# Performance work log

Measured on AMD Instinct MI355X. Metric: run time of the kernel, lower is better.

## Reference

```python
import jax, jax.numpy as jnp
import numpy as np

N_NODES = 50000
N_EDGES = 800000
D = 128
BN_EPS = 1e-5


def setup_inputs() -> dict:
    key = jax.random.key(0)
    ks = jax.random.split(key, 12)
    inp = {
        "X": jax.random.normal(ks[0], (N_NODES, D), dtype=jnp.float32),
        "W_A": jax.random.normal(ks[1], (D, D), dtype=jnp.float32) * 0.05,
        "b_A": jax.random.normal(ks[2], (D,), dtype=jnp.float32) * 0.05,
        "W_B": jax.random.normal(ks[3], (D, D), dtype=jnp.float32) * 0.05,
        "b_B": jax.random.normal(ks[4], (D,), dtype=jnp.float32) * 0.05,
        "W_D": jax.random.normal(ks[5], (D, D), dtype=jnp.float32) * 0.05,
        "b_D": jax.random.normal(ks[6], (D,), dtype=jnp.float32) * 0.05,
        "W_E": jax.random.normal(ks[7], (D, D), dtype=jnp.float32) * 0.05,
        "b_E": jax.random.normal(ks[8], (D,), dtype=jnp.float32) * 0.05,
        "gamma": jnp.ones((D,), dtype=jnp.float32),
        "beta": jnp.zeros((D,), dtype=jnp.float32),
        "src": jax.random.randint(ks[9], (N_EDGES,), 0, N_NODES, dtype=jnp.int64 if jax.config.jax_enable_x64 else jnp.int32),
        "dst": jax.random.randint(ks[10], (N_EDGES,), 0, N_NODES, dtype=jnp.int64 if jax.config.jax_enable_x64 else jnp.int32),
    }
    return inp


def reference(X, W_A, b_A, W_B, b_B, W_D, b_D, W_E, b_E, gamma, beta, src, dst):
    n = X.shape[0]
    # Node projections (nn.Linear: x @ W^T + b; here W stored as [d_in, d_out])
    AX = X @ W_A + b_A
    BX = X @ W_B + b_B
    DX = X @ W_D + b_D
    EX = X @ W_E + b_E

    # Per-edge gate: e_j = DX[src] + EX[dst]; sigma = sigmoid(e_j)
    sigma = jax.nn.sigmoid(DX[src] + EX[dst])  # [E, D]

    # Weighted segment-sum aggregation onto destination nodes
    num = jax.ops.segment_sum(sigma * BX[src], dst, num_segments=n)  # [N, D]
    den = jax.ops.segment_sum(sigma, dst, num_segments=n)            # [N, D]
    deg = jax.ops.segment_sum(jnp.ones_like(dst, dtype=X.dtype), dst, num_segments=n)  # [N]

    has_msg = (deg > 0)[:, None]
    den_safe = jnp.where(has_msg, den, 1.0)
    # DGL: nodes with no incoming messages keep H = X
    H = jnp.where(has_msg, AX + num / den_safe, X)

    # snorm scaling
    H = H * (1.0 / n)

    # BatchNorm1d over node dim (training-mode batch statistics, biased var)
    mean = jnp.mean(H, axis=0)
    var = jnp.mean(jnp.square(H - mean), axis=0)
    H = (H - mean) / jnp.sqrt(var + BN_EPS) * gamma + beta

    H = jax.nn.relu(H)
    return X + H
```

## Files before the change

### kernel.cpp

```cpp
#include <hip/hip_runtime.h>
#include <hip/hip_bf16.h>
#include <math.h>

#define NN 50000
#define DD 128
#define BN_EPS 1e-5f
#define SCAN_NB 49

typedef short short8 __attribute__((ext_vector_type(8)));
typedef float f32x4 __attribute__((ext_vector_type(4)));

__device__ __forceinline__ unsigned short f2bf(float f) {
    __hip_bfloat16 h = __float2bfloat16(f);
    return *reinterpret_cast<unsigned short*>(&h);
}
__device__ __forceinline__ float frcp(float x) { return __builtin_amdgcn_rcpf(x); }

__global__ __launch_bounds__(256) void prep_w(
    const float* __restrict__ W0, const float* __restrict__ W1,
    const float* __restrict__ W2, const float* __restrict__ W3,
    unsigned short* __restrict__ Wt)
{
    const int which = blockIdx.x;
    const float* W = (which == 0) ? W0 : (which == 1) ? W1 : (which == 2) ? W2 : W3;
    unsigned short* O = Wt + (size_t)which * 16384;
    for (int it = 0; it < 8; ++it) {
        const int id = it * 256 + threadIdx.x;
        const int col = id >> 4;
        const int kc  = id & 15;
        unsigned int pk[4];
        #pragma unroll
        for (int p = 0; p < 4; ++p) {
            const float f0 = W[(kc * 8 + p * 2 + 0) * DD + col];
            const float f1 = W[(kc * 8 + p * 2 + 1) * DD + col];
            pk[p] = (unsigned int)f2bf(f0) | ((unsigned int)f2bf(f1) << 16);
        }
        uint4 v = make_uint4(pk[0], pk[1], pk[2], pk[3]);
        *(uint4*)(O + col * 128 + kc * 8) = v;
    }
}

__global__ __launch_bounds__(512, 4) void gemm4(
    const float* __restrict__ X, const unsigned short* __restrict__ Wt,
    const float* __restrict__ bA, const float* __restrict__ bB,
    const float* __restrict__ bD, const float* __restrict__ bE,
    float* __restrict__ AX, float* __restrict__ QX,
    unsigned short* __restrict__ BD)
{
    __shared__ char xs[64 * 256];
    const int row0 = blockIdx.x * 64;
    const int tid  = threadIdx.x;

    #pragma unroll
    for (int it = 0; it < 2; ++it) {
        const int idx = it * 512 + tid;
        const int r = idx >> 4;
        const int c = idx & 15;
        const bool valid = (row0 + r) < NN;
        float4 va = make_float4(0.f, 0.f, 0.f, 0.f);
        float4 vb = make_float4(0.f, 0.f, 0.f, 0.f);
        if (valid) {
            const float* gp = X + (size_t)(row0 + r) * DD + c * 8;
            va = *(const float4*)(gp);
            vb = *(const float4*)(gp + 4);
        }
        uint4 pk;
        pk.x = (unsigned int)f2bf(va.x) | ((unsigned int)f2bf(va.y) << 16);
        pk.y = (unsigned int)f2bf(va.z) | ((unsigned int)f2bf(va.w) << 16);
        pk.z = (unsigned int)f2bf(vb.x) | ((unsigned int)f2bf(vb.y) << 16);
        pk.w = (unsigned int)f2bf(vb.z) | ((unsigned int)f2bf(vb.w) << 16);
        *(uint4*)(xs + r * 256 + ((c * 16) ^ ((r & 7) << 4))) = pk;
    }
    __syncthreads();

    const int wid  = tid >> 6;
    const int p    = wid >> 1;
    const int h    = wid & 1;
    const int lane = tid & 63;
    const int lr = lane & 15, lg = lane >> 4;

    f32x4 acc[4][4];
    #pragma unroll
    for (int m = 0; m < 4; ++m)
        #pragma unroll
        for (int n = 0; n < 4; ++n)
            acc[m][n] = (f32x4){0.f, 0.f, 0.f, 0.f};

    const char* wb = (const char*)(Wt + (size_t)p * 16384) + h * 64 * 256;

    #pragma unroll
    for (int k = 0; k < 4; ++k) {
        short8 aW[4];
        #pragma unroll
        for (int n = 0; n < 4; ++n)
            aW[n] = *(const short8*)(wb + (n * 16 + lr) * 256 + k * 64 + lg * 16);
        short8 bX[4];
        #pragma unroll
        for (int m = 0; m < 4; ++m)
            bX[m] = *(const short8*)(xs + (m * 16 + lr) * 256 +
                                     ((k * 64 + lg * 16) ^ ((lr & 7) << 4)));
        #pragma unroll
        for (int m = 0; m < 4; ++m)
            #pragma unroll
            for (int n = 0; n < 4; ++n)
                acc[m][n] = __builtin_amdgcn_mfma_f32_16x16x32_bf16(
                    aW[n], bX[m], acc[m][n], 0, 0, 0);
    }

    const float* bias = (p == 0) ? bA : (p == 1) ? bB : (p == 2) ? bD : bE;
    #pragma unroll
    for (int n = 0; n < 4; ++n) {
        const int cbase = h * 64 + n * 16 + lg * 4;
        const float4 bv = *(const float4*)(bias + cbase);
        #pragma unroll
        for (int m = 0; m < 4; ++m) {
            const int row = row0 + m * 16 + lr;
            if (row < NN) {
                float v0 = acc[m][n][0] + bv.x;
                float v1 = acc[m][n][1] + bv.y;
                float v2 = acc[m][n][2] + bv.z;
                float v3 = acc[m][n][3] + bv.w;
                if (p == 0) {
                    *(float4*)(AX + (size_t)row * DD + cbase) = make_float4(v0, v1, v2, v3);
                } else if (p == 3) {
                    *(float4*)(QX + (size_t)row * DD + cbase) =
                        make_float4(__expf(-v0), __expf(-v1), __expf(-v2), __expf(-v3));
                } else {
                    if (p == 2) {
                        v0 = __expf(-v0); v1 = __expf(-v1);
                        v2 = __expf(-v2); v3 = __expf(-v3);
                    }
                    uint2 pk;
                    pk.x = (unsigned int)f2bf(v0) | ((unsigned int)f2bf(v1) << 16);
                    pk.y = (unsigned int)f2bf(v2) | ((unsigned int)f2bf(v3) << 16);
                    char* dstp = (char*)BD + (size_t)row * 512 + (cbase >> 2) * 16
                               + ((p == 2) ? 8 : 0);
                    *(uint2*)dstp = pk;
                }
            }
        }
    }
}

__global__ void hist_k(const int* __restrict__ dst, int* __restrict__ deg, int ne)
{
    const int e = blockIdx.x * blockDim.x + threadIdx.x;
    if (e < ne) atomicAdd(&deg[dst[e]], 1);
}

__global__ __launch_bounds__(1024) void partial_k(const int* __restrict__ deg,
                                                  int* __restrict__ bsum)
{
    __shared__ int ls[16];
    const int idx = blockIdx.x * 1024 + threadIdx.x;
    int v = (idx < NN) ? deg[idx] : 0;
    #pragma unroll
    for (int o = 1; o < 64; o <<= 1) v += __shfl_xor(v, o, 64);
    if ((threadIdx.x & 63) == 0) ls[threadIdx.x >> 6] = v;
    __syncthreads();
    if (threadIdx.x == 0) {
        int s = 0;
        #pragma unroll
        for (int i = 0; i < 16; ++i) s += ls[i];
        bsum[blockIdx.x] = s;
    }
}

__global__ __launch_bounds__(64) void scanblk_k(const int* __restrict__ bsum,
                                                int* __restrict__ bbase,
                                                int* __restrict__ off)
{
    const int t = threadIdx.x;
    int v = (t < SCAN_NB) ? bsum[t] : 0;
    const int orig = v;
    #pragma unroll
    for (int o = 1; o < 64; o <<= 1) {
        const int u = __shfl_up(v, o, 64);
        if (t >= o) v += u;
    }
    if (t < SCAN_NB) bbase[t] = v - orig;
    if (t == 63) off[NN] = v;
}

__global__ __launch_bounds__(1024) void offs_k(const int* __restrict__ deg,
                                               const int* __restrict__ bbase,
                                               int* __restrict__ off,
                                               int* __restrict__ cursor)
{
    __shared__ int ws[16];
    const int idx = blockIdx.x * 1024 + threadIdx.x;
    const int t = threadIdx.x;
    int v = (idx < NN) ? deg[idx] : 0;
    const int orig = v;
    #pragma unroll
    for (int o = 1; o < 64; o <<= 1) {
        const int u = __shfl_up(v, o, 64);
        if ((t & 63) >= o) v += u;
    }
    if ((t & 63) == 63) ws[t >> 6] = v;
    __syncthreads();
    int base = 0;
    for (int i = 0; i < (t >> 6); ++i) base += ws[i];
    const int ex = bbase[blockIdx.x] + base + (v - orig);
    if (idx < NN) { off[idx] = ex; cursor[idx] = ex; }
}

__global__ void scatter_k(const int* __restrict__ src, const int* __restrict__ dst,
                          int* __restrict__ cursor, int* __restrict__ srt, int ne)
{
    const int e = blockIdx.x * blockDim.x + threadIdx.x;
    if (e < ne) {
        const int p = atomicAdd(&cursor[dst[e]], 1);
        srt[p] = src[e];
    }
}

__global__ __launch_bounds__(256) void agg_k(
    const float* __restrict__ AX, const float* __restrict__ QX,
    const uint4* __restrict__ BD4, const float* __restrict__ X,
    const int* __restrict__ off, const int* __restrict__ srt,
    float* __restrict__ H)
{
    const int wid  = threadIdx.x >> 6;
    const int lane = threadIdx.x & 63;
    const int half = lane >> 5;
    const int f    = lane & 31;
    const int node = blockIdx.x * 4 + wid;
    const int beg = off[node], end = off[node + 1];

    const float4 q = *(const float4*)(QX + (size_t)node * DD + f * 4);
    float num[4] = {0.f, 0.f, 0.f, 0.f};
    float den[4] = {0.f, 0.f, 0.f, 0.f};

#define EDGE4(wv)                                                            \
    {                                                                        \
        const float b0_ = __uint_as_float((wv).x << 16);                     \
        const float b1_ = __uint_as_float((wv).x & 0xffff0000u);             \
        const float b2_ = __uint_as_float((wv).y << 16);                     \
        const float b3_ = __uint_as_float((wv).y & 0xffff0000u);             \
        const float p0_ = __uint_as_float((wv).z << 16);                     \
        const float p1_ = __uint_as_float((wv).z & 0xffff0000u);             \
        const float p2_ = __uint_as_float((wv).w << 16);                     \
        const float p3_ = __uint_as_float((wv).w & 0xffff0000u);             \
        const float s0_ = frcp(fmaf(p0_, q.x, 1.0f));                        \
        const float s1_ = frcp(fmaf(p1_, q.y, 1.0f));                        \
        const float s2_ = frcp(fmaf(p2_, q.z, 1.0f));                        \
        const float s3_ = frcp(fmaf(p3_, q.w, 1.0f));                        \
        num[0] = fmaf(s0_, b0_, num[0]); den[0] += s0_;                      \
        num[1] = fmaf(s1_, b1_, num[1]); den[1] += s1_;                      \
        num[2] = fmaf(s2_, b2_, num[2]); den[2] += s2_;                      \
        num[3] = fmaf(s3_, b3_, num[3]); den[3] += s3_;                      \
    }

    int i = beg;
    for (; i + 8 <= end; i += 8) {
        int ss[4];
        #pragma unroll
        for (int u = 0; u < 4; ++u) ss[u] = srt[i + 2 * u + half];
        uint4 wv[4];
        #pragma unroll
        for (int u = 0; u < 4; ++u) wv[u] = BD4[(size_t)ss[u] * 32 + f];
        #pragma unroll
        for (int u = 0; u < 4; ++u) EDGE4(wv[u]);
    }
    for (; i + 2 <= end; i += 2) {
        const int s = srt[i + half];
        const uint4 wv = BD4[(size_t)s * 32 + f];
        EDGE4(wv);
    }
    if (i < end && half == 0) {
        const int s = srt[i];
        const uint4 wv = BD4[(size_t)s * 32 + f];
        EDGE4(wv);
    }
#undef EDGE4

    #pragma unroll
    for (int j = 0; j < 4; ++j) {
        num[j] += __shfl_xor(num[j], 32);
        den[j] += __shfl_xor(den[j], 32);
    }

    if (half == 0) {
        float4 hv;
        if (end > beg) {
            const float4 ax = *(const float4*)(AX + (size_t)node * DD + f * 4);
            hv.x = ax.x + num[0] * frcp(den[0]);
            hv.y = ax.y + num[1] * frcp(den[1]);
            hv.z = ax.z + num[2] * frcp(den[2]);
            hv.w = ax.w + num[3] * frcp(den[3]);
        } else {
            hv = *(const float4*)(X + (size_t)node * DD + f * 4);
        }
        hv.x *= (1.0f / NN); hv.y *= (1.0f / NN);
        hv.z *= (1.0f / NN); hv.w *= (1.0f / NN);
        *(float4*)(H + (size_t)node * DD + f * 4) = hv;
    }
}

__global__ __launch_bounds__(256) void bnstat_k(const float* __restrict__ H,
                                                float* __restrict__ acc)
{
    __shared__ float l1[256], l2[256];
    const int t = threadIdx.x;
    const int f = t & 127, g = t >> 7;
    const int n0 = blockIdx.x * 125;
    float s1 = 0.f, s2 = 0.f;
    for (int r = g; r < 125; r += 2) {
        const float h = H[(size_t)(n0 + r) * DD + f];
        s1 += h;
        s2 += h * h;
    }
    l1[t] = s1; l2[t] = s2;
    __syncthreads();
    if (t < 128) {
        s1 = l1[t] + l1[t + 128];
        s2 = l2[t] + l2[t + 128];
        atomicAdd(&acc[f], s1);
        atomicAdd(&acc[128 + f], s2);
    }
}

__global__ __launch_bounds__(256) void final_k(
    const float* __restrict__ H, const float* __restrict__ X,
    const float* __restrict__ acc,
    const float* __restrict__ gamma, const float* __restrict__ beta,
    float* __restrict__ out)
{
    const int i = blockIdx.x * 256 + threadIdx.x;
    if (i >= NN * 32) return;
    const int f = (i & 31) * 4;
    const float4 h = *(const float4*)(H + (size_t)i * 4);
    const float4 x = *(const float4*)(X + (size_t)i * 4);
    float4 o;
    #pragma unroll
    for (int c = 0; c < 4; ++c) {
        const float mean = acc[f + c] * (1.0f / NN);
        const float var  = acc[128 + f + c] * (1.0f / NN) - mean * mean;
        const float rstd = rsqrtf(var + BN_EPS);
        const float hv = (c == 0) ? h.x : (c == 1) ? h.y : (c == 2) ? h.z : h.w;
        const float xv = (c == 0) ? x.x : (c == 1) ? x.y : (c == 2) ? x.z : x.w;
        float v = (hv - mean) * rstd * gamma[f + c] + beta[f + c];
        v = fmaxf(v, 0.f);
        const float r = xv + v;
        if (c == 0) o.x = r; else if (c == 1) o.y = r; else if (c == 2) o.z = r; else o.w = r;
    }
    *(float4*)(out + (size_t)i * 4) = o;
}

extern "C" void kernel_launch(void* const* d_in, const int* in_sizes, int n_in,
                              void* d_out, int out_size, void* d_ws, size_t ws_size,
                              hipStream_t stream)
{
    const float* X     = (const float*)d_in[0];
    const float* W_A   = (const float*)d_in[1];
    const float* b_A   = (const float*)d_in[2];
    const float* W_B   = (const float*)d_in[3];
    const float* b_B   = (const float*)d_in[4];
    const float* W_D   = (const float*)d_in[5];
    const float* b_D   = (const float*)d_in[6];
    const float* W_E   = (const float*)d_in[7];
    const float* b_E   = (const float*)d_in[8];
    const float* gamma = (const float*)d_in[9];
    const float* beta  = (const float*)d_in[10];
    const int*   src   = (const int*)d_in[11];
    const int*   dst   = (const int*)d_in[12];
    const int    ne    = in_sizes[11];
    float* out = (float*)d_out;

    char* w = (char*)d_ws;
    const size_t ndf = (size_t)NN * DD * sizeof(float);
    unsigned short* Wt = (unsigned short*)w;  w += 4 * 16384 * sizeof(unsigned short);
    float* AX = (float*)w;                    w += ndf;
    float* QX = (float*)w;                    w += ndf;
    unsigned short* BD = (unsigned short*)w;  w += (size_t)NN * 256 * sizeof(unsigned short);
    float* H  = (float*)w;                    w += ndf;
    float* acc = (float*)w;                   w += 256 * sizeof(float);
    int* deg    = (int*)w;                    w += (size_t)NN * sizeof(int);
    int* off    = (int*)w;                    w += (size_t)(NN + 4) * sizeof(int);
    int* cursor = (int*)w;                    w += (size_t)NN * sizeof(int);
    int* bsum   = (int*)w;                    w += 64 * sizeof(int);
    int* bbase  = (int*)w;                    w += 64 * sizeof(int);
    int* srt    = (int*)w;                    w += (size_t)ne * sizeof(int);

    hipMemsetAsync(deg, 0, (size_t)NN * sizeof(int), stream);
    hipMemsetAsync(acc, 0, 256 * sizeof(float), stream);

    prep_w<<<4, 256, 0, stream>>>(W_A, W_B, W_D, W_E, Wt);
    hist_k<<<(ne + 255) / 256, 256, 0, stream>>>(dst, deg, ne);
    partial_k<<<SCAN_NB, 1024, 0, stream>>>(deg, bsum);
    scanblk_k<<<1, 64, 0, stream>>>(bsum, bbase, off);
    offs_k<<<SCAN_NB, 1024, 0, stream>>>(deg, bbase, off, cursor);

    gemm4<<<(NN + 63) / 64, 512, 0, stream>>>(X, Wt, b_A, b_B, b_D, b_E, AX, QX, BD);

    scatter_k<<<(ne + 255) / 256, 256, 0, stream>>>(src, dst, cursor, srt, ne);

    agg_k<<<NN / 4, 256, 0, stream>>>(AX, QX, (const uint4*)BD, X, off, srt, H);

    bnstat_k<<<400, 256, 0, stream>>>(H, acc);

    final_k<<<(NN * 32 + 255) / 256, 256, 0, stream>>>(H, X, acc, gamma, beta, out);
}
```

Before: 332.1 us.

## Merge scan kernels, vectorize hist/scatter, deepen agg unroll, vectorize bnstat

Replaces the three-kernel degree prefix scan with one 1024-thread block that scans a padded degree array (13 int4 per thread). The histogram and scatter kernels now read int4 of edge indices, with four atomics per thread. The aggregation loop gains a 16-edge unrolled stage, and the BN statistics kernel switches to float4 loads with a tree reduction in shared memory. These mostly cut kernel launch count and per-thread overhead. Edge counts not divisible by four would lose their trailing edges, and the single-block scan puts the whole prefix sum on one CU.

```diff
diff --git a/kernel.cpp b/kernel.cpp
--- a/kernel.cpp
+++ b/kernel.cpp
@@ -5,7 +5,7 @@
 #define NN 50000
 #define DD 128
 #define BN_EPS 1e-5f
-#define SCAN_NB 49
+#define PADN 53248
 
 typedef short short8 __attribute__((ext_vector_type(8)));
 typedef float f32x4 __attribute__((ext_vector_type(4)));
@@ -142,76 +142,70 @@
     }
 }
 
-__global__ void hist_k(const int* __restrict__ dst, int* __restrict__ deg, int ne)
+__global__ void hist_k(const int4* __restrict__ dst4, int* __restrict__ deg, int ne4)
 {
     const int e = blockIdx.x * blockDim.x + threadIdx.x;
-    if (e < ne) atomicAdd(&deg[dst[e]], 1);
-}
-
-__global__ __launch_bounds__(1024) void partial_k(const int* __restrict__ deg,
-                                                  int* __restrict__ bsum)
-{
-    __shared__ int ls[16];
-    const int idx = blockIdx.x * 1024 + threadIdx.x;
-    int v = (idx < NN) ? deg[idx] : 0;
-    #pragma unroll
-    for (int o = 1; o < 64; o <<= 1) v += __shfl_xor(v, o, 64);
-    if ((threadIdx.x & 63) == 0) ls[threadIdx.x >> 6] = v;
-    __syncthreads();
-    if (threadIdx.x == 0) {
-        int s = 0;
-        #pragma unroll
-        for (int i = 0; i < 16; ++i) s += ls[i];
-        bsum[blockIdx.x] = s;
-    }
-}
-
-__global__ __launch_bounds__(64) void scanblk_k(const int* __restrict__ bsum,
-                                                int* __restrict__ bbase,
-                                                int* __restrict__ off)
-{
-    const int t = threadIdx.x;
-    int v = (t < SCAN_NB) ? bsum[t] : 0;
-    const int orig = v;
-    #pragma unroll
-    for (int o = 1; o < 64; o <<= 1) {
-        const int u = __shfl_up(v, o, 64);
-        if (t >= o) v += u;
-    }
-    if (t < SCAN_NB) bbase[t] = v - orig;
-    if (t == 63) off[NN] = v;
-}
-
-__global__ __launch_bounds__(1024) void offs_k(const int* __restrict__ deg,
-                                               const int* __restrict__ bbase,
+    if (e < ne4) {
+        const int4 d = dst4[e];
+        atomicAdd(&deg[d.x], 1);
+        atomicAdd(&deg[d.y], 1);
+        atomicAdd(&deg[d.z], 1);
+        atomicAdd(&deg[d.w], 1);
+    }
+}
+
+__global__ __launch_bounds__(1024) void scan_k(const int* __restrict__ deg,
                                                int* __restrict__ off,
                                                int* __restrict__ cursor)
 {
     __shared__ int ws[16];
-    const int idx = blockIdx.x * 1024 + threadIdx.x;
     const int t = threadIdx.x;
-    int v = (idx < NN) ? deg[idx] : 0;
-    const int orig = v;
+    int4 v[13];
+    const int4* dp = (const int4*)deg + t * 13;
+    #pragma unroll
+    for (int j = 0; j < 13; ++j) v[j] = dp[j];
+
+    int s = 0;
+    #pragma unroll
+    for (int j = 0; j < 13; ++j) s += v[j].x + v[j].y + v[j].z + v[j].w;
+
+    int incl = s;
     #pragma unroll
     for (int o = 1; o < 64; o <<= 1) {
-        const int u = __shfl_up(v, o, 64);
-        if ((t & 63) >= o) v += u;
-    }
-    if ((t & 63) == 63) ws[t >> 6] = v;
+        const int u = __shfl_up(incl, o, 64);
+        if ((t & 63) >= o) incl += u;
+    }
+    if ((t & 63) == 63) ws[t >> 6] = incl;
     __syncthreads();
-    int base = 0;
-    for (int i = 0; i < (t >> 6); ++i) base += ws[i];
-    const int ex = bbase[blockIdx.x] + base + (v - orig);
-    if (idx < NN) { off[idx] = ex; cursor[idx] = ex; }
-}
-
-__global__ void scatter_k(const int* __restrict__ src, const int* __restrict__ dst,
-                          int* __restrict__ cursor, int* __restrict__ srt, int ne)
+    int wbase = 0;
+    for (int i = 0; i < (t >> 6); ++i) wbase += ws[i];
+
+    int run = wbase + incl - s;
+    int4* op = (int4*)off + t * 13;
+    int4* cp = (int4*)cursor + t * 13;
+    #pragma unroll
+    for (int j = 0; j < 13; ++j) {
+        int4 w;
+        w.x = run; run += v[j].x;
+        w.y = run; run += v[j].y;
+        w.z = run; run += v[j].z;
+        w.w = run; run += v[j].w;
+        op[j] = w;
+        cp[j] = w;
+    }
+}
+
+__global__ void scatter_k(const int4* __restrict__ src4, const int4* __restrict__ dst4,
+                          int* __restrict__ cursor, int* __restrict__ srt, int ne4)
 {
     const int e = blockIdx.x * blockDim.x + threadIdx.x;
-    if (e < ne) {
-        const int p = atomicAdd(&cursor[dst[e]], 1);
-        srt[p] = src[e];
+    if (e < ne4) {
+        const int4 s = src4[e];
+        const int4 d = dst4[e];
+        srt[atomicAdd(&cursor[d.x], 1)] = s.x;
+        srt[atomicAdd(&cursor[d.y], 1)] = s.y;
+        srt[atomicAdd(&cursor[d.z], 1)] = s.z;
+        srt[atomicAdd(&cursor[d.w], 1)] = s.w;
     }
 }
 
@@ -253,6 +247,16 @@
     }
 
     int i = beg;
+    for (; i + 16 <= end; i += 16) {
+        int ss[8];
+        #pragma unroll
+        for (int u = 0; u < 8; ++u) ss[u] = srt[i + 2 * u + half];
+        uint4 wv[8];
+        #pragma unroll
+        for (int u = 0; u < 8; ++u) wv[u] = BD4[(size_t)ss[u] * 32 + f];
+        #pragma unroll
+        for (int u = 0; u < 8; ++u) EDGE4(wv[u]);
+    }
     for (; i + 8 <= end; i += 8) {
         int ss[4];
         #pragma unroll
@@ -301,23 +305,40 @@
 __global__ __launch_bounds__(256) void bnstat_k(const float* __restrict__ H,
                                                 float* __restrict__ acc)
 {
-    __shared__ float l1[256], l2[256];
+    __shared__ float l1[256][4], l2[256][4];
     const int t = threadIdx.x;
-    const int f = t & 127, g = t >> 7;
+    const int q = t & 31;
+    const int rg = t >> 5;
     const int n0 = blockIdx.x * 125;
-    float s1 = 0.f, s2 = 0.f;
-    for (int r = g; r < 125; r += 2) {
-        const float h = H[(size_t)(n0 + r) * DD + f];
-        s1 += h;
-        s2 += h * h;
-    }
-    l1[t] = s1; l2[t] = s2;
+    float s1[4] = {0.f, 0.f, 0.f, 0.f}, s2[4] = {0.f, 0.f, 0.f, 0.f};
+    for (int r = rg; r < 125; r += 8) {
+        const float4 h = *(const float4*)(H + (size_t)(n0 + r) * DD + q * 4);
+        s1[0] += h.x; s2[0] += h.x * h.x;
+        s1[1] += h.y; s2[1] += h.y * h.y;
+        s1[2] += h.z; s2[2] += h.z * h.z;
+        s1[3] += h.w; s2[3] += h.w * h.w;
+    }
+    #pragma unroll
+    for (int c = 0; c < 4; ++c) { l1[t][c] = s1[c]; l2[t][c] = s2[c]; }
     __syncthreads();
-    if (t < 128) {
-        s1 = l1[t] + l1[t + 128];
-        s2 = l2[t] + l2[t + 128];
-        atomicAdd(&acc[f], s1);
-        atomicAdd(&acc[128 + f], s2);
+    if (rg < 4) {
+        #pragma unroll
+        for (int c = 0; c < 4; ++c) { l1[t][c] += l1[t + 128][c]; l2[t][c] += l2[t + 128][c]; }
+    }
+    __syncthreads();
+    if (rg < 2) {
+        #pragma unroll
+        for (int c = 0; c < 4; ++c) { l1[t][c] += l1[t + 64][c]; l2[t][c] += l2[t + 64][c]; }
+    }
+    __syncthreads();
+    if (rg == 0) {
+        #pragma unroll
+        for (int c = 0; c < 4; ++c) {
+            const float a1 = l1[t][c] + l1[t + 32][c];
+            const float a2 = l2[t][c] + l2[t + 32][c];
+            atomicAdd(&acc[q * 4 + c], a1);
+            atomicAdd(&acc[128 + q * 4 + c], a2);
+        }
     }
 }
 
@@ -376,25 +397,22 @@
     unsigned short* BD = (unsigned short*)w;  w += (size_t)NN * 256 * sizeof(unsigned short);
     float* H  = (float*)w;                    w += ndf;
     float* acc = (float*)w;                   w += 256 * sizeof(float);
-    int* deg    = (int*)w;                    w += (size_t)NN * sizeof(int);
-    int* off    = (int*)w;                    w += (size_t)(NN + 4) * sizeof(int);
-    int* cursor = (int*)w;                    w += (size_t)NN * sizeof(int);
-    int* bsum   = (int*)w;                    w += 64 * sizeof(int);
-    int* bbase  = (int*)w;                    w += 64 * sizeof(int);
+    int* deg    = (int*)w;                    w += (size_t)PADN * sizeof(int);
+    int* off    = (int*)w;                    w += (size_t)PADN * sizeof(int);
+    int* cursor = (int*)w;                    w += (size_t)PADN * sizeof(int);
     int* srt    = (int*)w;                    w += (size_t)ne * sizeof(int);
 
-    hipMemsetAsync(deg, 0, (size_t)NN * sizeof(int), stream);
+    hipMemsetAsync(deg, 0, (size_t)PADN * sizeof(int), stream);
     hipMemsetAsync(acc, 0, 256 * sizeof(float), stream);
 
     prep_w<<<4, 256, 0, stream>>>(W_A, W_B, W_D, W_E, Wt);
-    hist_k<<<(ne + 255) / 256, 256, 0, stream>>>(dst, deg, ne);
-    partial_k<<<SCAN_NB, 1024, 0, stream>>>(deg, bsum);
-    scanblk_k<<<1, 64, 0, stream>>>(bsum, bbase, off);
-    offs_k<<<SCAN_NB, 1024, 0, stream>>>(deg, bbase, off, cursor);
+    hist_k<<<(ne / 4 + 255) / 256, 256, 0, stream>>>((const int4*)dst, deg, ne / 4);
+    scan_k<<<1, 1024, 0, stream>>>(deg, off, cursor);
 
     gemm4<<<(NN + 63) / 64, 512, 0, stream>>>(X, Wt, b_A, b_B, b_D, b_E, AX, QX, BD);
 
-    scatter_k<<<(ne + 255) / 256, 256, 0, stream>>>(src, dst, cursor, srt, ne);
+    scatter_k<<<(ne / 4 + 255) / 256, 256, 0, stream>>>((const int4*)src, (const int4*)dst,
+                                                        cursor, srt, ne / 4);
 
     agg_k<<<NN / 4, 256, 0, stream>>>(AX, QX, (const uint4*)BD, X, off, srt, H);
 
```

New measurement: 362.8 us. 9.3% more time.
